# Kernel tuning notes

Hardware: AMD Instinct MI355X
Metric: run time of the kernel (lower is better)

The kernel has to match this reference:

```python
import jax, jax.numpy as jnp
import numpy as np


def _lenet(x, cw1, cb1, cw2, cb2, fw1, fb1, fw2, fb2, fw3, fb3):
    # x: [B,1,28,28] -> [B,10] softmax probs (Conv -> MaxPool -> ReLU, twice)
    y = jax.lax.conv_general_dilated(x, cw1, (1, 1), 'VALID') + cb1[None, :, None, None]
    y = jax.lax.reduce_window(y, -jnp.inf, jax.lax.max, (1, 1, 2, 2), (1, 1, 2, 2), 'VALID')
    y = jax.nn.relu(y)
    y = jax.lax.conv_general_dilated(y, cw2, (1, 1), 'VALID') + cb2[None, :, None, None]
    y = jax.lax.reduce_window(y, -jnp.inf, jax.lax.max, (1, 1, 2, 2), (1, 1, 2, 2), 'VALID')
    y = jax.nn.relu(y)
    y = y.reshape(y.shape[0], -1)  # [B, 16*4*4]
    y = jax.nn.relu(y @ fw1.T + fb1)
    y = jax.nn.relu(y @ fw2.T + fb2)
    return jax.nn.softmax(y @ fw3.T + fb3, axis=1)


def setup_inputs() -> dict:
    key = jax.random.key(0)
    ks = jax.random.split(key, 11)
    B = 16384
    inp = {
        'x': jax.random.normal(ks[0], (B, 2, 28, 28), dtype=jnp.float32),
        'cw1': jax.random.normal(ks[1], (6, 1, 5, 5), dtype=jnp.float32) * 0.2,
        'cb1': jax.random.normal(ks[2], (6,), dtype=jnp.float32) * 0.1,
        'cw2': jax.random.normal(ks[3], (16, 6, 5, 5), dtype=jnp.float32) * 0.08,
        'cb2': jax.random.normal(ks[4], (16,), dtype=jnp.float32) * 0.1,
        'fw1': jax.random.normal(ks[5], (120, 256), dtype=jnp.float32) * 0.0625,
        'fb1': jax.random.normal(ks[6], (120,), dtype=jnp.float32) * 0.05,
        'fw2': jax.random.normal(ks[7], (84, 120), dtype=jnp.float32) * 0.09,
        'fb2': jax.random.normal(ks[8], (84,), dtype=jnp.float32) * 0.05,
        'fw3': jax.random.normal(ks[9], (10, 84), dtype=jnp.float32) * 0.1,
        'fb3': jax.random.normal(ks[10], (10,), dtype=jnp.float32) * 0.05,
    }
    return inp


def reference(x, cw1, cb1, cw2, cb2, fw1, fb1, fw2, fb2, fw3, fb3):
    p1 = _lenet(x[:, 0:1], cw1, cb1, cw2, cb2, fw1, fb1, fw2, fb2, fw3, fb3)  # [B,10]
    p2 = _lenet(x[:, 1:2], cw1, cb1, cw2, cb2, fw1, fb1, fw2, fb2, fw3, fb3)  # [B,10]
    # torch Conv1d with weight=flip(p2[i]) and padding=K-1 is the full linear
    # convolution z[t] = sum_j p2[j] * p1[t-j], length 2*10-1 = 19.
    # p2 is treated as a constant (copied under no_grad in the original).
    p2c = jax.lax.stop_gradient(p2)
    Z = jax.vmap(lambda a, b: jnp.convolve(a, b, mode='full'))(p1, p2c)  # [B,19]
    return jnp.log(Z)
```

## Files before the change

kernel.cpp:

```cpp
#include <hip/hip_runtime.h>
#include <math.h>


#define SPB 4
#define P1H_IN 440
#define P1H_IC 144

typedef _Float16 f16x2 __attribute__((ext_vector_type(2)));
typedef _Float16 half4 __attribute__((ext_vector_type(4)));
typedef _Float16 half8 __attribute__((ext_vector_type(8)));
typedef float floatx4 __attribute__((ext_vector_type(4)));
typedef float floatx16 __attribute__((ext_vector_type(16)));

#define WS_F2  8192
#define WS_C1B 11264
#define WS_C2A 11456
#define WS_C2K 11776
#define WS_TOT 12096

__global__ __launch_bounds__(256) void prep_ws(
    const float* __restrict__ fw1, const float* __restrict__ fw2,
    const float* __restrict__ cw1, const float* __restrict__ cw2,
    uint4* __restrict__ ws)
{
    int idx = blockIdx.x * 256 + threadIdx.x;
    if (idx >= WS_TOT) return;
    if (idx < WS_F2) {
        int l = idx & 63, ks = (idx >> 6) & 15, ot = idx >> 10;
        int cn = l & 15, g = l >> 4;
        int o = ot * 16 + cn, k0 = ks * 16 + g * 4;
        union { uint4 u; _Float16 h[8]; } r;
        for (int j = 0; j < 4; ++j) {
            float w = (o < 120) ? fw1[o * 256 + k0 + j] : 0.f;
            r.h[2 * j] = (_Float16)w; r.h[2 * j + 1] = r.h[2 * j];
        }
        ws[idx] = r.u;
    } else if (idx < WS_C1B) {
        int e = idx - WS_F2;
        int l = e & 63, ks = (e >> 6) & 7, ot = e >> 9;
        int cn = l & 15, g = l >> 4;
        int o = ot * 16 + cn, k0 = ks * 16 + g * 4;
        union { uint4 u; _Float16 h[8]; } r;
        for (int j = 0; j < 4; ++j) {
            float w = (o < 84 && k0 + j < 120) ? fw2[o * 120 + k0 + j] : 0.f;
            r.h[2 * j] = (_Float16)w; r.h[2 * j + 1] = r.h[2 * j];
        }
        ws[idx] = r.u;
    } else if (idx < WS_C2A) {
        int e = idx - WS_C1B; int l = e & 63; int ks = e >> 6;
        int l5 = l >> 5, cn = l & 31, s = cn >> 3, ch = cn & 7;
        int ky = 2 * ks + l5;
        union { uint4 u; _Float16 h[8]; } r;
        for (int j = 0; j < 8; ++j) {
            int kx = j - s;
            float w = (ch < 6 && ky < 5 && kx >= 0 && kx <= 4)
                    ? cw1[ch * 25 + ky * 5 + kx] : 0.f;
            r.h[j] = (_Float16)w;
        }
        ws[idx] = r.u;
    } else if (idx < WS_C2K) {
        int e = idx - WS_C2A; int l = e & 63; int ks = e >> 6;
        int cn = l & 15, g = l >> 4;
        union { uint4 u; _Float16 h[8]; } r;
        for (int j = 0; j < 8; ++j) {
            int hidx = ks * 32 + g * 8 + j;
            int kp = hidx >> 1, el = hidx & 1;
            float w = 0.f;
            if (kp < 75) {
                int icp = kp / 25, rr = kp % 25;
                w = cw2[cn * 150 + (2 * icp + el) * 25 + rr];
            }
            r.h[j] = (_Float16)w;
        }
        ws[idx] = r.u;
    } else {
        int e = idx - WS_C2K; int l = e & 63; int ks = e >> 6;
        int g = l >> 4;
        union { uint4 u; int i[4]; } r;
        for (int j = 0; j < 4; ++j) {
            int kp = ks * 16 + g * 4 + j;
            kp = kp > 74 ? 74 : kp;
            int icp = kp / 25, rr = kp % 25, ky = rr / 5, kx = rr % 5;
            r.i[j] = icp * P1H_IC + ky * 12 + kx;
        }
        ws[idx] = r.u;
    }
}

#define P2H_BASE(n) (((n) & 3) * 784 + (((n) >> 2) & 1) * 260)
#define F1H_BASE(n) (((n) & 3) * 784 + 520 + (((n) >> 2) & 1) * 132)

__global__ __launch_bounds__(256, 5) void lenet_fused(
    const float* __restrict__ x,
    const float* __restrict__ cb1,
    const float* __restrict__ cb2,
    const float* __restrict__ fb1,
    const float* __restrict__ fb2,
    const float* __restrict__ fw3,
    const float* __restrict__ fb3,
    const uint4* __restrict__ ws4,
    float* __restrict__ out)
{
    const int tid = threadIdx.x;
    const int b0  = blockIdx.x * SPB;

    __shared__ __align__(16) float s_pool[3888];
    __shared__ __align__(16) f16x2 s_p1h [8 * P1H_IN];

    uint32_t* s_u32 = (uint32_t*)s_pool;
    float* s_log = s_pool + 3808;

    const int lane = tid & 63;
    const int wv   = tid >> 6;

    {
        const int l5   = lane >> 5;
        const int cn   = lane & 31;
        const int s    = cn >> 3;
        const int ch   = cn & 7;
        const int Y0   = cn < 24 ? cn : 23;

        half8 bfr[3];
#pragma unroll
        for (int ks = 0; ks < 3; ++ks) {
            union { uint4 u; half8 h; } t;
            t.u = ws4[WS_C1B + ks * 64 + lane];
            bfr[ks] = t.h;
        }
        const float bch = (ch < 6) ? cb1[ch] : 0.f;
        const bool  wrl = ((s & 1) == 0) && (ch < 6);
        _Float16* p1w = (_Float16*)s_p1h;
        _Float16* ipbase = (_Float16*)(s_u32 + wv * 784);

        floatx16 zero16 = {0.f,0.f,0.f,0.f, 0.f,0.f,0.f,0.f,
                           0.f,0.f,0.f,0.f, 0.f,0.f,0.f,0.f};

#pragma unroll 1
        for (int p = 0; p < 2; ++p) {
            {
                const float4* xi = (const float4*)(x + (size_t)b0 * 1568)
                                 + (wv + 4 * p) * 196;
                ushort4* sh = (ushort4*)ipbase;
                for (int i = lane; i < 196; i += 64) {
                    float4 q = xi[i];
                    union { ushort4 u; _Float16 h[4]; } w;
                    w.h[0] = (_Float16)q.x; w.h[1] = (_Float16)q.y;
                    w.h[2] = (_Float16)q.z; w.h[3] = (_Float16)q.w;
                    sh[i] = w.u;
                }
            }
            asm volatile("s_waitcnt lgkmcnt(0)" ::: "memory");

            const int inst = wv + 4 * p;
            const int wb = (inst * P1H_IN + (ch >> 1) * P1H_IC) * 2 + (ch & 1);

#pragma unroll 1
            for (int c = 0; c < 3; ++c) {
                floatx16 acc0 = zero16, acc1 = zero16;
#pragma unroll
                for (int ks = 0; ks < 3; ++ks) {
                    int ra = Y0 + 2 * ks + l5;
                    ra = ra > 27 ? 27 : ra;
                    const _Float16* rp = ipbase + ra * 28 + c * 8;
                    union { half8 h8; half4 h4[2]; } a0, a1;
                    a0.h4[0] = *(const half4*)(rp);
                    a0.h4[1] = *(const half4*)(rp + 4);
                    a1.h4[0] = a0.h4[1];
                    a1.h4[1] = *(const half4*)(rp + 8);
                    acc0 = __builtin_amdgcn_mfma_f32_32x32x16_f16(
                        a0.h8, bfr[ks], acc0, 0, 0, 0);
                    acc1 = __builtin_amdgcn_mfma_f32_32x32x16_f16(
                        a1.h8, bfr[ks], acc1, 0, 0, 0);
                }
#pragma unroll
                for (int h = 0; h < 2; ++h) {
                    const int xbi = 2 * c + h;
                    const int px2 = (xbi * 2 + (s >> 1)) * 2;
#pragma unroll
                    for (int d = 0; d < 4; ++d) {
#pragma unroll
                        for (int cp = 0; cp < 2; ++cp) {
                            float e0 = h ? acc1[4 * d + 2 * cp]
                                         : acc0[4 * d + 2 * cp];
                            float e1 = h ? acc1[4 * d + 2 * cp + 1]
                                         : acc0[4 * d + 2 * cp + 1];
                            float vy = fmaxf(e0, e1);
                            float vo = __shfl_xor(vy, 8);
                            float vp = fmaxf(vy, vo);
                            float r  = fmaxf(vp + bch, 0.f);
                            int  py  = cp + 4 * d + 2 * l5;
                            if (wrl && py < 12)
                                p1w[wb + py * 24 + px2] = (_Float16)r;
                        }
                    }
                }
            }
        }
    }
    asm volatile("s_waitcnt lgkmcnt(0)" ::: "memory");

    {
        const int g  = lane >> 4;
        const int cn = lane & 15;

        half8 afr[5];
        int4  kot[5];
#pragma unroll
        for (int ks = 0; ks < 5; ++ks) {
            union { uint4 u; half8 h; } t;
            t.u = ws4[WS_C2A + ks * 64 + lane];
            afr[ks] = t.h;
            union { uint4 u; int4 i; } k;
            k.u = ws4[WS_C2K + ks * 64 + lane];
            kot[ks] = k.i;
        }

        float bias4[4];
#pragma unroll
        for (int r = 0; r < 4; ++r) bias4[r] = cb2[g * 4 + r];

        const int csb = (cn >> 3) * 12 + (cn & 7);
        const int px = (lane & 7) >> 1;
        const bool wrp = (lane & 9) == 0;

        floatx4 zero4 = {0.f, 0.f, 0.f, 0.f};

#pragma unroll 1
        for (int ih = 0; ih < 2; ++ih) {
            const int inst = wv + 4 * ih;
            const f16x2* pb = s_p1h + inst * P1H_IN + csb;

            floatx4 acc[4] = {zero4, zero4, zero4, zero4};
#pragma unroll
            for (int ks = 0; ks < 5; ++ks) {
                const int k0 = kot[ks].x, k1 = kot[ks].y,
                          k2 = kot[ks].z, k3 = kot[ks].w;
#pragma unroll
                for (int ntl = 0; ntl < 4; ++ntl) {
                    union { half8 h8; f16x2 h2[4]; } bp;
                    bp.h2[0] = pb[k0 + 24 * ntl];
                    bp.h2[1] = pb[k1 + 24 * ntl];
                    bp.h2[2] = pb[k2 + 24 * ntl];
                    bp.h2[3] = pb[k3 + 24 * ntl];
                    acc[ntl] = __builtin_amdgcn_mfma_f32_16x16x32_f16(
                        afr[ks], bp.h8, acc[ntl], 0, 0, 0);
                }
            }

            uint32_t* p2o = s_u32 + P2H_BASE(inst) + px;
#pragma unroll
            for (int ntl = 0; ntl < 4; ++ntl) {
#pragma unroll
                for (int r = 0; r < 4; ++r) {
                    float v = acc[ntl][r];
                    v = fmaxf(v, __shfl_xor(v, 1));
                    v = fmaxf(v, __shfl_xor(v, 8));
                    v = fmaxf(v + bias4[r], 0.f);
                    _Float16 hi = (_Float16)v;
                    _Float16 lo = (_Float16)(v - (float)hi);
                    f16x2 pr; pr.x = hi; pr.y = lo;
                    if (wrp) p2o[(g * 4 + r) * 16 + ntl * 4] =
                        __builtin_bit_cast(uint32_t, pr);
                }
            }
        }
    }
    __syncthreads();

    {
        const int cn = lane & 15, g4 = lane >> 4;
        const uint4* apb4 = (const uint4*)(s_u32 + P2H_BASE(cn & 7));
        const uint4* bw0 = ws4 + (size_t)wv * 1024 + lane;
        const uint4* bw1 = ws4 + (size_t)(wv + 4) * 1024 + lane;
        floatx4 acc0 = {0.f,0.f,0.f,0.f}, acc1 = {0.f,0.f,0.f,0.f};
#pragma unroll 4
        for (int ks = 0; ks < 16; ++ks) {
            union { half8 h; uint4 u; } af;
            af.u = apb4[ks * 4 + g4];
            union { half8 h; uint4 u; } b0, b1;
            b0.u = bw0[ks * 64]; b1.u = bw1[ks * 64];
            acc0 = __builtin_amdgcn_mfma_f32_16x16x32_f16(af.h, b0.h, acc0, 0,0,0);
            acc1 = __builtin_amdgcn_mfma_f32_16x16x32_f16(af.h, b1.h, acc1, 0,0,0);
        }
#pragma unroll
        for (int t = 0; t < 2; ++t) {
            int o = (wv + 4 * t) * 16 + cn;
            floatx4 a = t ? acc1 : acc0;
            float bias = (o < 120) ? fb1[o] : 0.f;
            if (g4 < 2) {
#pragma unroll
                for (int r = 0; r < 4; ++r) {
                    int inst = g4 * 4 + r;
                    float v = fmaxf(a[r] + bias, 0.f);
                    if (o >= 120) v = 0.f;
                    _Float16 hi = (_Float16)v;
                    _Float16 lo = (_Float16)(v - (float)hi);
                    f16x2 pr; pr.x = hi; pr.y = lo;
                    s_u32[F1H_BASE(inst) + o] = __builtin_bit_cast(uint32_t, pr);
                }
            }
        }
    }
    __syncthreads();

    {
        const int cn = lane & 15, g4 = lane >> 4;
        const uint4* apb4 = (const uint4*)(s_u32 + F1H_BASE(cn & 7));
        const uint4* bw0 = ws4 + WS_F2 + (size_t)wv * 512 + lane;
        const uint4* bw1 = bw0 + 2048;
        const bool has1 = wv < 2;
        floatx4 acc0 = {0.f,0.f,0.f,0.f}, acc1 = {0.f,0.f,0.f,0.f};
#pragma unroll 4
        for (int ks = 0; ks < 8; ++ks) {
            union { half8 h; uint4 u; } af;
            af.u = apb4[ks * 4 + g4];
            union { half8 h; uint4 u; } b0;
            b0.u = bw0[ks * 64];
            acc0 = __builtin_amdgcn_mfma_f32_16x16x32_f16(af.h, b0.h, acc0, 0,0,0);
            if (has1) {
                union { half8 h; uint4 u; } b1;
                b1.u = bw1[ks * 64];
                acc1 = __builtin_amdgcn_mfma_f32_16x16x32_f16(af.h, b1.h, acc1, 0,0,0);
            }
        }
        float* s_f2 = (float*)(s_u32 + 3136);
#pragma unroll
        for (int t = 0; t < 2; ++t) {
            if (t && !has1) break;
            int o = (wv + 4 * t) * 16 + cn;
            floatx4 a = t ? acc1 : acc0;
            if (o < 84 && g4 < 2) {
                float bias = fb2[o];
#pragma unroll
                for (int r = 0; r < 4; ++r) {
                    int inst = g4 * 4 + r;
                    s_f2[inst * 84 + o] = fmaxf(a[r] + bias, 0.f);
                }
            }
        }
    }
    __syncthreads();

    if (tid < 80) {
        int o    = tid % 10;
        int inst = tid / 10;
        const float4* wr = (const float4*)(fw3 + o * 84);
        const float4* q0 = (const float4*)(s_pool + 3136 + inst * 84);
        float a0 = 0.f;
#pragma unroll
        for (int k = 0; k < 21; ++k) {
            float4 w4 = wr[k];
            float4 p = q0[k];
            a0 = fmaf(w4.x,p.x,a0); a0 = fmaf(w4.y,p.y,a0); a0 = fmaf(w4.z,p.z,a0); a0 = fmaf(w4.w,p.w,a0);
        }
        s_log[inst * 10 + o] = a0 + fb3[o];
    }
    __syncthreads();

    if (tid < 19 * SPB) {
        int ls = tid / 19;
        int t  = tid % 19;
        const float* la = &s_log[(ls * 2 + 0) * 10];
        const float* lb = &s_log[(ls * 2 + 1) * 10];
        float pa[10], pb[10];
        float mxa = la[0], mxb = lb[0];
#pragma unroll
        for (int j = 1; j < 10; ++j) { mxa = fmaxf(mxa, la[j]); mxb = fmaxf(mxb, lb[j]); }
        float sa = 0.f, sb = 0.f;
#pragma unroll
        for (int j = 0; j < 10; ++j) {
            pa[j] = __expf(la[j] - mxa); sa += pa[j];
            pb[j] = __expf(lb[j] - mxb); sb += pb[j];
        }
        float inv = 1.f / (sa * sb);
        int jlo = t - 9 > 0 ? t - 9 : 0;
        int jhi = t < 9 ? t : 9;
        float z = 0.f;
        for (int j = jlo; j <= jhi; ++j)
            z += pa[j] * pb[t - j];
        out[(size_t)(b0 + ls) * 19 + t] = __logf(z * inv);
    }
}

extern "C" void kernel_launch(void* const* d_in, const int* in_sizes, int n_in,
                              void* d_out, int out_size, void* d_ws, size_t ws_size,
                              hipStream_t stream) {
    const float* x   = (const float*)d_in[0];
    const float* cw1 = (const float*)d_in[1];
    const float* cb1 = (const float*)d_in[2];
    const float* cw2 = (const float*)d_in[3];
    const float* cb2 = (const float*)d_in[4];
    const float* fw1 = (const float*)d_in[5];
    const float* fb1 = (const float*)d_in[6];
    const float* fw2 = (const float*)d_in[7];
    const float* fb2 = (const float*)d_in[8];
    const float* fw3 = (const float*)d_in[9];
    const float* fb3 = (const float*)d_in[10];
    float* out = (float*)d_out;
    uint4* ws4 = (uint4*)d_ws;

    const int B = in_sizes[0] / (2 * 28 * 28);

    prep_ws<<<(WS_TOT + 255) / 256, 256, 0, stream>>>(fw1, fw2, cw1, cw2, ws4);
    lenet_fused<<<B / SPB, 256, 0, stream>>>(x, cb1, cb2,
                                             fb1, fb2, fw3, fb3, ws4, out);
}
```

Baseline: 250.7 us.

## Process eight samples per block and prefetch next input into registers

Doubles samples per block from 4 to 8 so the FC-layer MFMAs use all 16 rows of the 16x16 tiles instead of wasting half. Reuses the conv1 output buffer for pool2 and fc1 activations, shrinks the input staging area, and prefetches the next image into registers while the current one is converted and convolved. Shared memory grows and the occupancy hint drops from 5 to 4 blocks per CU, and register pressure rises from the prefetch buffers.

```diff
diff --git a/kernel.cpp b/kernel.cpp
--- a/kernel.cpp
+++ b/kernel.cpp
@@ -2,7 +2,7 @@
 #include <math.h>
 
 
-#define SPB 4
+#define SPB 8
 #define P1H_IN 440
 #define P1H_IC 144
 
@@ -87,10 +87,7 @@
     }
 }
 
-#define P2H_BASE(n) (((n) & 3) * 784 + (((n) >> 2) & 1) * 260)
-#define F1H_BASE(n) (((n) & 3) * 784 + 520 + (((n) >> 2) & 1) * 132)
-
-__global__ __launch_bounds__(256, 5) void lenet_fused(
+__global__ __launch_bounds__(256, 4) void lenet_fused(
     const float* __restrict__ x,
     const float* __restrict__ cb1,
     const float* __restrict__ cb2,
@@ -104,11 +101,12 @@
     const int tid = threadIdx.x;
     const int b0  = blockIdx.x * SPB;
 
-    __shared__ __align__(16) float s_pool[3888];
-    __shared__ __align__(16) f16x2 s_p1h [8 * P1H_IN];
+    __shared__ __align__(16) float s_pool[3072];
+    __shared__ __align__(16) f16x2 s_p1h [16 * P1H_IN];
 
     uint32_t* s_u32 = (uint32_t*)s_pool;
-    float* s_log = s_pool + 3808;
+    uint32_t* p1u   = (uint32_t*)s_p1h;
+    float* s_log = s_pool + 2912;
 
     const int lane = tid & 63;
     const int wv   = tid >> 6;
@@ -130,28 +128,45 @@
         const float bch = (ch < 6) ? cb1[ch] : 0.f;
         const bool  wrl = ((s & 1) == 0) && (ch < 6);
         _Float16* p1w = (_Float16*)s_p1h;
-        _Float16* ipbase = (_Float16*)(s_u32 + wv * 784);
+        _Float16* ipbase = (_Float16*)(s_u32 + wv * 392);
+        const float4* xbase = (const float4*)(x + (size_t)b0 * 1568);
 
         floatx16 zero16 = {0.f,0.f,0.f,0.f, 0.f,0.f,0.f,0.f,
                            0.f,0.f,0.f,0.f, 0.f,0.f,0.f,0.f};
 
+        float4 qreg[4];
+#pragma unroll
+        for (int j = 0; j < 4; ++j) {
+            int i = j * 64 + lane;
+            if (i < 196) qreg[j] = xbase[wv * 196 + i];
+        }
+
 #pragma unroll 1
-        for (int p = 0; p < 2; ++p) {
+        for (int p = 0; p < 4; ++p) {
+            const int inst = wv + 4 * p;
             {
-                const float4* xi = (const float4*)(x + (size_t)b0 * 1568)
-                                 + (wv + 4 * p) * 196;
                 ushort4* sh = (ushort4*)ipbase;
-                for (int i = lane; i < 196; i += 64) {
-                    float4 q = xi[i];
-                    union { ushort4 u; _Float16 h[4]; } w;
-                    w.h[0] = (_Float16)q.x; w.h[1] = (_Float16)q.y;
-                    w.h[2] = (_Float16)q.z; w.h[3] = (_Float16)q.w;
-                    sh[i] = w.u;
+#pragma unroll
+                for (int j = 0; j < 4; ++j) {
+                    int i = j * 64 + lane;
+                    if (i < 196) {
+                        float4 q = qreg[j];
+                        union { ushort4 u; _Float16 h[4]; } w;
+                        w.h[0] = (_Float16)q.x; w.h[1] = (_Float16)q.y;
+                        w.h[2] = (_Float16)q.z; w.h[3] = (_Float16)q.w;
+                        sh[i] = w.u;
+                    }
+                }
+            }
+            if (p < 3) {
+#pragma unroll
+                for (int j = 0; j < 4; ++j) {
+                    int i = j * 64 + lane;
+                    if (i < 196) qreg[j] = xbase[(inst + 4) * 196 + i];
                 }
             }
             asm volatile("s_waitcnt lgkmcnt(0)" ::: "memory");
 
-            const int inst = wv + 4 * p;
             const int wb = (inst * P1H_IN + (ch >> 1) * P1H_IC) * 2 + (ch & 1);
 
 #pragma unroll 1
@@ -226,7 +241,7 @@
         floatx4 zero4 = {0.f, 0.f, 0.f, 0.f};
 
 #pragma unroll 1
-        for (int ih = 0; ih < 2; ++ih) {
+        for (int ih = 0; ih < 4; ++ih) {
             const int inst = wv + 4 * ih;
             const f16x2* pb = s_p1h + inst * P1H_IN + csb;
 
@@ -247,7 +262,7 @@
                 }
             }
 
-            uint32_t* p2o = s_u32 + P2H_BASE(inst) + px;
+            uint32_t* p2o = p1u + inst * 440 + px;
 #pragma unroll
             for (int ntl = 0; ntl < 4; ++ntl) {
 #pragma unroll
@@ -269,7 +284,7 @@
 
     {
         const int cn = lane & 15, g4 = lane >> 4;
-        const uint4* apb4 = (const uint4*)(s_u32 + P2H_BASE(cn & 7));
+        const uint4* apb4 = (const uint4*)(p1u + cn * 440);
         const uint4* bw0 = ws4 + (size_t)wv * 1024 + lane;
         const uint4* bw1 = ws4 + (size_t)(wv + 4) * 1024 + lane;
         floatx4 acc0 = {0.f,0.f,0.f,0.f}, acc1 = {0.f,0.f,0.f,0.f};
@@ -287,17 +302,15 @@
             int o = (wv + 4 * t) * 16 + cn;
             floatx4 a = t ? acc1 : acc0;
             float bias = (o < 120) ? fb1[o] : 0.f;
-            if (g4 < 2) {
-#pragma unroll
-                for (int r = 0; r < 4; ++r) {
-                    int inst = g4 * 4 + r;
-                    float v = fmaxf(a[r] + bias, 0.f);
-                    if (o >= 120) v = 0.f;
-                    _Float16 hi = (_Float16)v;
-                    _Float16 lo = (_Float16)(v - (float)hi);
-                    f16x2 pr; pr.x = hi; pr.y = lo;
-                    s_u32[F1H_BASE(inst) + o] = __builtin_bit_cast(uint32_t, pr);
-                }
+#pragma unroll
+            for (int r = 0; r < 4; ++r) {
+                int inst = g4 * 4 + r;
+                float v = fmaxf(a[r] + bias, 0.f);
+                if (o >= 120) v = 0.f;
+                _Float16 hi = (_Float16)v;
+                _Float16 lo = (_Float16)(v - (float)hi);
+                f16x2 pr; pr.x = hi; pr.y = lo;
+                p1u[inst * 440 + 264 + o] = __builtin_bit_cast(uint32_t, pr);
             }
         }
     }
@@ -305,7 +318,7 @@
 
     {
         const int cn = lane & 15, g4 = lane >> 4;
-        const uint4* apb4 = (const uint4*)(s_u32 + F1H_BASE(cn & 7));
+        const uint4* apb4 = (const uint4*)(p1u + cn * 440 + 264);
         const uint4* bw0 = ws4 + WS_F2 + (size_t)wv * 512 + lane;
         const uint4* bw1 = bw0 + 2048;
         const bool has1 = wv < 2;
@@ -323,13 +336,13 @@
                 acc1 = __builtin_amdgcn_mfma_f32_16x16x32_f16(af.h, b1.h, acc1, 0,0,0);
             }
         }
-        float* s_f2 = (float*)(s_u32 + 3136);
+        float* s_f2 = (float*)(s_u32 + 1568);
 #pragma unroll
         for (int t = 0; t < 2; ++t) {
             if (t && !has1) break;
             int o = (wv + 4 * t) * 16 + cn;
             floatx4 a = t ? acc1 : acc0;
-            if (o < 84 && g4 < 2) {
+            if (o < 84) {
                 float bias = fb2[o];
 #pragma unroll
                 for (int r = 0; r < 4; ++r) {
@@ -341,11 +354,11 @@
     }
     __syncthreads();
 
-    if (tid < 80) {
+    if (tid < 160) {
         int o    = tid % 10;
         int inst = tid / 10;
         const float4* wr = (const float4*)(fw3 + o * 84);
-        const float4* q0 = (const float4*)(s_pool + 3136 + inst * 84);
+        const float4* q0 = (const float4*)(s_pool + 1568 + inst * 84);
         float a0 = 0.f;
 #pragma unroll
         for (int k = 0; k < 21; ++k) {
```

After: 224.4 us. 10.5% less time.
